# Kernel tuning notes

Hardware: AMD Instinct MI355X
Metric: run time of the kernel (lower is better)

Reference implementation:

```python
import jax, jax.numpy as jnp
import numpy as np

N, E = 50000, 1600000
IN_DIM, HID, L, H = 300, 256, 3, 4
HD = HID // H  # 64
EPS = 1e-5


def setup_inputs() -> dict:
    key = jax.random.key(0)
    ks = jax.random.split(key, 24)
    s = 0.02
    inp = {
        'node_feats': jax.random.normal(ks[0], (N, IN_DIM), jnp.float32),
        'role': jax.random.randint(ks[1], (N,), 0, 3),
        'edge_src': jax.random.randint(ks[2], (E,), 0, N),
        'edge_dst': jax.random.randint(ks[3], (E,), 0, N),
        'edge_weights': jax.random.uniform(ks[4], (E,), jnp.float32),
        # input role transforms (question / entity / context)
        'Wq': jax.random.normal(ks[5], (IN_DIM, HID), jnp.float32) * s,
        'bq': jnp.zeros((HID,), jnp.float32),
        'We': jax.random.normal(ks[6], (IN_DIM, HID), jnp.float32) * s,
        'be': jnp.zeros((HID,), jnp.float32),
        'Wc': jax.random.normal(ks[7], (IN_DIM, HID), jnp.float32) * s,
        'bc': jnp.zeros((HID,), jnp.float32),
        # per-head value projections [H, HID, HD] (q/k projections omitted:
        # softmax over a scalar == 1.0, so they never affect output or grads)
        'Wv': jax.random.normal(ks[8], (H, HID, HD), jnp.float32) * s,
        'bv': jnp.zeros((H, HD), jnp.float32),
        # shared 'default' edge-type transform (the torch code always falls
        # through to 'default' because edata['rel'] entries are tensors)
        'Wd': jax.random.normal(ks[9], (HD, HD), jnp.float32) * s,
        'bd': jnp.zeros((HD,), jnp.float32),
        # attention_output
        'Wo': jax.random.normal(ks[10], (HID, HID), jnp.float32) * s,
        'bo': jnp.zeros((HID,), jnp.float32),
        # GRUCell params (torch layout: [3*HID, in], gate order r,z,n)
        'W_ih': jax.random.normal(ks[11], (3 * HID, HID), jnp.float32) * s,
        'W_hh': jax.random.normal(ks[12], (3 * HID, HID), jnp.float32) * s,
        'b_ih': jnp.zeros((3 * HID,), jnp.float32),
        'b_hh': jnp.zeros((3 * HID,), jnp.float32),
        # per-layer LayerNorm affine params [L, HID]
        'ln_w': jnp.ones((L, HID), jnp.float32),
        'ln_b': jnp.zeros((L, HID), jnp.float32),
    }
    return inp


def _layernorm(x, w, b):
    mu = jnp.mean(x, -1, keepdims=True)
    var = jnp.mean(jnp.square(x - mu), -1, keepdims=True)
    return (x - mu) * jax.lax.rsqrt(var + EPS) * w + b


def _gru_cell(x, hprev, W_ih, W_hh, b_ih, b_hh):
    gi = x @ W_ih.T + b_ih
    gh = hprev @ W_hh.T + b_hh
    i_r, i_z, i_n = jnp.split(gi, 3, axis=-1)
    h_r, h_z, h_n = jnp.split(gh, 3, axis=-1)
    r = jax.nn.sigmoid(i_r + h_r)
    z = jax.nn.sigmoid(i_z + h_z)
    n = jnp.tanh(i_n + r * h_n)
    return (1.0 - z) * n + z * hprev


def reference(node_feats, role, edge_src, edge_dst, edge_weights,
              Wq, bq, We, be, Wc, bc, Wv, bv, Wd, bd, Wo, bo,
              W_ih, W_hh, b_ih, b_hh, ln_w, ln_b):
    n_nodes = node_feats.shape[0]
    # role-dependent input transform: 0=question, 1=evidence/answer, 2=other
    hq = node_feats @ Wq + bq
    he = node_feats @ We + be
    hc = node_feats @ Wc + bc
    r = role[:, None]
    h = jax.nn.relu(jnp.where(r == 0, hq, jnp.where(r == 1, he, hc)))

    path_mem = jax.lax.stop_gradient(h)  # .detach().clone()
    prev_h = h
    num_layers, num_heads = ln_w.shape[0], Wv.shape[0]
    for layer in range(num_layers):
        head_msgs = []
        for hd in range(num_heads):
            # value proj + shared 'default' edge transform (node-level, fused)
            vt = (h @ Wv[hd] + bv[hd]) @ Wd + bd  # [N, HD]
            # scalar softmax == 1.0 -> attn_weight == edge_weight
            msg = vt[edge_src] * edge_weights[:, None]  # [E, HD]
            head_msgs.append(jax.ops.segment_sum(msg, edge_dst,
                                                 num_segments=n_nodes))
        combined = jnp.concatenate(head_msgs, axis=-1)  # [N, HID]
        path_mem = _gru_cell(combined, path_mem, W_ih, W_hh, b_ih, b_hh)
        h = _layernorm(prev_h + combined @ Wo + bo, ln_w[layer], ln_b[layer])
        # dropout: identity in eval mode
        prev_h = h
    return h + path_mem
```

## Files before the change

### kernel.cpp

```cpp
#include <hip/hip_runtime.h>
#include <math.h>

#define NN 50000
#define EE 1600000
#define IND 300
#define KPAD 320
#define NL 3
#define NBLK 785

typedef unsigned short u16;
typedef __attribute__((ext_vector_type(8))) short short8;
typedef __attribute__((ext_vector_type(4))) float floatx4;

__device__ __forceinline__ float b2f(u16 u) {
  union { unsigned i; float f; } v; v.i = ((unsigned)u) << 16; return v.f;
}
__device__ __forceinline__ u16 f2b(float f) {
  union { unsigned i; float f; } v; v.f = f;
  unsigned b = v.i; b += 0x7fffu + ((b >> 16) & 1u);
  return (u16)(b >> 16);
}
__device__ __forceinline__ float sigf(float x) { return 1.0f / (1.0f + __expf(-x)); }

__global__ void count_kernel(const int* __restrict__ dst, int* __restrict__ cnt) {
  int e = blockIdx.x * 256 + threadIdx.x;
  if (e < EE) atomicAdd(&cnt[dst[e]], 1);
}

__global__ void scan_kernel(const int* __restrict__ cnt, int* __restrict__ rs) {
  __shared__ int wsum[16], wpre[16];
  __shared__ int carryS, totS;
  const int t = threadIdx.x;
  const int l = t & 63, wid = t >> 6;
  if (t == 0) carryS = 0;
  __syncthreads();
  for (int base = 0; base < NN; base += 1024) {
    const int carry = carryS;
    const int i = base + t;
    int v = (i < NN) ? cnt[i] : 0;
    int x = v;
    #pragma unroll
    for (int off = 1; off < 64; off <<= 1) {
      int y = __shfl_up(x, off);
      if (l >= off) x += y;
    }
    if (l == 63) wsum[wid] = x;
    __syncthreads();
    if (t < 16) {
      int s = wsum[t];
      int xx = s;
      #pragma unroll
      for (int off = 1; off < 16; off <<= 1) {
        int y = __shfl_up(xx, off);
        if (t >= off) xx += y;
      }
      wpre[t] = xx - s;
      if (t == 15) totS = xx;
    }
    __syncthreads();
    if (i < NN) rs[i] = carry + wpre[wid] + (x - v);
    __syncthreads();
    if (t == 0) carryS = carry + totS;
    __syncthreads();
  }
  if (t == 0) rs[NN] = carryS;
}

__global__ void fill_kernel(const int* __restrict__ dst, const int* __restrict__ rs,
                            int* __restrict__ ncnt, const int* __restrict__ esrc,
                            const float* __restrict__ ew, int2* __restrict__ srcw) {
  int e = blockIdx.x * 256 + threadIdx.x;
  if (e < EE) {
    int d = dst[e];
    int p = atomicAdd(&ncnt[d], 1);
    int2 v;
    v.x = esrc[e];
    v.y = __float_as_int(ew[e]);
    srcw[rs[d] + p] = v;
  }
}

__global__ void role_count(const int* __restrict__ role, int* __restrict__ cnt3) {
  __shared__ int lc[3];
  if (threadIdx.x < 3) lc[threadIdx.x] = 0;
  __syncthreads();
  int i = blockIdx.x * 256 + threadIdx.x;
  if (i < NN) atomicAdd(&lc[role[i]], 1);
  __syncthreads();
  if (threadIdx.x < 3) atomicAdd(&cnt3[threadIdx.x], lc[threadIdx.x]);
}

__global__ void role_plan(const int* __restrict__ cnt3, int* __restrict__ pbase,
                          int* __restrict__ blkrole) {
  __shared__ int pb[4];
  if (threadIdx.x == 0) {
    pb[0] = 0;
    for (int b = 0; b < 3; ++b) pb[b + 1] = pb[b] + (((cnt3[b] + 63) >> 6) << 6);
    for (int b = 0; b < 4; ++b) pbase[b] = pb[b];
  }
  __syncthreads();
  for (int blk = threadIdx.x; blk < NBLK; blk += 256) {
    int m0 = blk * 64;
    int r = -1;
    for (int b = 0; b < 3; ++b)
      if (m0 >= pb[b] && m0 < pb[b + 1]) r = b;
    blkrole[blk] = r;
  }
}

__global__ void role_fill(const int* __restrict__ role, const int* __restrict__ pbase,
                          int* __restrict__ pos3, int* __restrict__ perm) {
  __shared__ int lcnt[3], lbase[3];
  int i = blockIdx.x * 256 + threadIdx.x;
  if (threadIdx.x < 3) lcnt[threadIdx.x] = 0;
  __syncthreads();
  int r = 0, lr = 0;
  bool valid = (i < NN);
  if (valid) {
    r = role[i];
    lr = atomicAdd(&lcnt[r], 1);
  }
  __syncthreads();
  if (threadIdx.x < 3) lbase[threadIdx.x] = atomicAdd(&pos3[threadIdx.x], lcnt[threadIdx.x]);
  __syncthreads();
  if (valid) perm[pbase[r] + lbase[r] + lr] = i;
}

__global__ void xcast_kernel(const float* __restrict__ X, u16* __restrict__ Xb) {
  size_t i = (size_t)blockIdx.x * 256 + threadIdx.x;
  if (i >= (size_t)NN * KPAD) return;
  int r = (int)(i / KPAD), k = (int)(i % KPAD);
  Xb[i] = (k < IND) ? f2b(X[(size_t)r * IND + k]) : (u16)0;
}

__global__ void wt3_kernel(const float* __restrict__ Wq, const float* __restrict__ We,
                           const float* __restrict__ Wc, u16* __restrict__ Wqt,
                           u16* __restrict__ Wet, u16* __restrict__ Wct) {
  int n = blockIdx.x;
  int which = blockIdx.y;
  const float* W = (which == 0) ? Wq : (which == 1) ? We : Wc;
  u16* Wt = (which == 0) ? Wqt : (which == 1) ? Wet : Wct;
  for (int k = threadIdx.x; k < KPAD; k += 256)
    Wt[(size_t)n * KPAD + k] = (k < IND) ? f2b(W[(size_t)k * 256 + n]) : (u16)0;
}

__global__ void wallt_kernel(const float* __restrict__ Wv, const float* __restrict__ Wd,
                             u16* __restrict__ Wallt) {
  int i = blockIdx.x;
  int c = threadIdx.x;
  int hd = c >> 6, j = c & 63;
  const float* wv = &Wv[hd * (256 * 64) + i * 64];
  float s = 0.f;
  #pragma unroll
  for (int m = 0; m < 64; ++m) s = fmaf(wv[m], Wd[m * 64 + j], s);
  Wallt[(size_t)c * 256 + i] = f2b(s);
}

__global__ void ball_kernel(const float* __restrict__ bv, const float* __restrict__ Wd,
                            const float* __restrict__ bd, float* __restrict__ ball) {
  int c = threadIdx.x;
  int hd = c >> 6, j = c & 63;
  float s = bd[j];
  #pragma unroll
  for (int m = 0; m < 64; ++m) s = fmaf(bv[hd * 64 + m], Wd[m * 64 + j], s);
  ball[c] = s;
}

__global__ void wot_kernel(const float* __restrict__ Wo, u16* __restrict__ Wot) {
  int n = blockIdx.x;
  int k = threadIdx.x;
  Wot[(size_t)n * 256 + k] = f2b(Wo[(size_t)k * 256 + n]);
}

__global__ void castbf2_kernel(const float* __restrict__ s0, const float* __restrict__ s1,
                               u16* __restrict__ d0, u16* __restrict__ d1) {
  int i = blockIdx.x * 256 + threadIdx.x;
  const int n = 768 * 256;
  if (i < n) d0[i] = f2b(s0[i]);
  else if (i < 2 * n) d1[i - n] = f2b(s1[i - n]);
}

#define GEMM_PROLOG \
  __shared__ __align__(16) u16 As[64][72]; \
  __shared__ __align__(16) u16 Bs[64][72]; \
  const int t = threadIdx.x; \
  const int lane = t & 63; \
  const int wv_ = t >> 6; \
  const int wr = wv_ >> 1, wc = wv_ & 1; \
  const int l15 = lane & 15, l4 = lane >> 4; \
  const int srow = t >> 2; \
  const int scol = (t & 3) << 4;

#define STAGE_A(AG, ASTRIDE, VALID, ROWIDX, K0) { \
  int4 v0 = {0, 0, 0, 0}, v1 = {0, 0, 0, 0}; \
  if (VALID) { \
    const int4* p_ = (const int4*)&(AG)[(size_t)(ROWIDX) * (ASTRIDE) + (K0) + scol]; \
    v0 = p_[0]; v1 = p_[1]; \
  } \
  *(int4*)&As[srow][scol] = v0; \
  *(int4*)&As[srow][scol + 8] = v1; }

#define STAGE_B(BG, BSTRIDE, ROWIDX, K0) { \
  const int4* p_ = (const int4*)&(BG)[(size_t)(ROWIDX) * (BSTRIDE) + (K0) + scol]; \
  *(int4*)&Bs[srow][scol] = p_[0]; \
  *(int4*)&Bs[srow][scol + 8] = p_[1]; }

#define MFMA_STEP(ACC) { \
  _Pragma("unroll") \
  for (int kc = 0; kc < 2; ++kc) { \
    short8 a0_ = *(const short8*)&As[wr * 32 + 0 + l15][kc * 32 + l4 * 8]; \
    short8 a1_ = *(const short8*)&As[wr * 32 + 16 + l15][kc * 32 + l4 * 8]; \
    short8 b0_ = *(const short8*)&Bs[wc * 32 + 0 + l15][kc * 32 + l4 * 8]; \
    short8 b1_ = *(const short8*)&Bs[wc * 32 + 16 + l15][kc * 32 + l4 * 8]; \
    ACC[0][0] = __builtin_amdgcn_mfma_f32_16x16x32_bf16(a0_, b0_, ACC[0][0], 0, 0, 0); \
    ACC[0][1] = __builtin_amdgcn_mfma_f32_16x16x32_bf16(a0_, b1_, ACC[0][1], 0, 0, 0); \
    ACC[1][0] = __builtin_amdgcn_mfma_f32_16x16x32_bf16(a1_, b0_, ACC[1][0], 0, 0, 0); \
    ACC[1][1] = __builtin_amdgcn_mfma_f32_16x16x32_bf16(a1_, b1_, ACC[1][1], 0, 0, 0); \
  } }

#define GEMM128_PROLOG \
  __shared__ __align__(16) u16 As[128][72]; \
  __shared__ __align__(16) u16 Bs[128][72]; \
  const int t = threadIdx.x; \
  const int lane = t & 63; \
  const int wv_ = t >> 6; \
  const int qr = (wv_ >> 1) * 64, qc = (wv_ & 1) * 64; \
  const int l15 = lane & 15, l4 = lane >> 4; \
  const int srow = t >> 1; \
  const int scol = (t & 1) * 32;

#define STAGE128_A(AG, ASTRIDE, VALID, ROWIDX, K0) { \
  int4 v0 = {0,0,0,0}, v1 = {0,0,0,0}, v2 = {0,0,0,0}, v3 = {0,0,0,0}; \
  if (VALID) { \
    const int4* p_ = (const int4*)&(AG)[(size_t)(ROWIDX) * (ASTRIDE) + (K0) + scol]; \
    v0 = p_[0]; v1 = p_[1]; v2 = p_[2]; v3 = p_[3]; \
  } \
  *(int4*)&As[srow][scol] = v0; *(int4*)&As[srow][scol + 8] = v1; \
  *(int4*)&As[srow][scol + 16] = v2; *(int4*)&As[srow][scol + 24] = v3; }

#define STAGE128_B(BG, BSTRIDE, ROWIDX, K0) { \
  const int4* p_ = (const int4*)&(BG)[(size_t)(ROWIDX) * (BSTRIDE) + (K0) + scol]; \
  *(int4*)&Bs[srow][scol] = p_[0]; *(int4*)&Bs[srow][scol + 8] = p_[1]; \
  *(int4*)&Bs[srow][scol + 16] = p_[2]; *(int4*)&Bs[srow][scol + 24] = p_[3]; }

#define MFMA128_STEP(ACC) { \
  _Pragma("unroll") \
  for (int kc = 0; kc < 2; ++kc) { \
    short8 af_[4], bf_[4]; \
    _Pragma("unroll") \
    for (int m = 0; m < 4; ++m) af_[m] = *(const short8*)&As[qr + m * 16 + l15][kc * 32 + l4 * 8]; \
    _Pragma("unroll") \
    for (int n = 0; n < 4; ++n) bf_[n] = *(const short8*)&Bs[qc + n * 16 + l15][kc * 32 + l4 * 8]; \
    _Pragma("unroll") \
    for (int m = 0; m < 4; ++m) \
      _Pragma("unroll") \
      for (int n = 0; n < 4; ++n) \
        ACC[m][n] = __builtin_amdgcn_mfma_f32_16x16x32_bf16(af_[m], bf_[n], ACC[m][n], 0, 0, 0); \
  } }

__global__ __launch_bounds__(256) void proj_mfma(
    const u16* __restrict__ Xb, const int* __restrict__ perm,
    const int* __restrict__ blkrole,
    const u16* __restrict__ Wqt, const u16* __restrict__ Wet, const u16* __restrict__ Wct,
    const float* __restrict__ bq, const float* __restrict__ be, const float* __restrict__ bc,
    u16* __restrict__ h, u16* __restrict__ pm) {
  const int brole = blkrole[blockIdx.y];
  if (brole < 0) return;
  GEMM_PROLOG
  const int m0 = blockIdx.y * 64;
  const int n0 = blockIdx.x * 64;
  const u16* Bt = (brole == 0) ? Wqt : (brole == 1) ? Wet : Wct;
  const float* bb = (brole == 0) ? bq : (brole == 1) ? be : bc;
  const int prow = perm[m0 + srow];
  floatx4 acc[2][2] = {};
  for (int k0 = 0; k0 < KPAD; k0 += 64) {
    STAGE_A(Xb, KPAD, prow >= 0, prow, k0)
    STAGE_B(Bt, KPAD, n0 + srow, k0)
    __syncthreads();
    MFMA_STEP(acc)
    __syncthreads();
  }
  #pragma unroll
  for (int m = 0; m < 2; ++m)
    #pragma unroll
    for (int reg = 0; reg < 4; ++reg) {
      int gr = m0 + wr * 32 + m * 16 + l4 * 4 + reg;
      int pr = perm[gr];
      if (pr >= 0) {
        #pragma unroll
        for (int n = 0; n < 2; ++n) {
          int c = n0 + wc * 32 + n * 16 + l15;
          float vo = fmaxf(acc[m][n][reg] + bb[c], 0.f);
          u16 ub = f2b(vo);
          h[(size_t)pr * 256 + c] = ub;
          pm[(size_t)pr * 256 + c] = ub;
        }
      }
    }
}

__global__ __launch_bounds__(256) void vgemm_mfma(
    const u16* __restrict__ A, const u16* __restrict__ Bt,
    const float* __restrict__ bias, u16* __restrict__ C) {
  GEMM128_PROLOG
  const int m0 = blockIdx.y * 128;
  const int n0 = blockIdx.x * 128;
  const int ar = m0 + srow;
  floatx4 acc[4][4] = {};
  for (int k0 = 0; k0 < 256; k0 += 64) {
    STAGE128_A(A, 256, ar < NN, ar, k0)
    STAGE128_B(Bt, 256, n0 + srow, k0)
    __syncthreads();
    MFMA128_STEP(acc)
    __syncthreads();
  }
  #pragma unroll
  for (int m = 0; m < 4; ++m)
    #pragma unroll
    for (int reg = 0; reg < 4; ++reg) {
      int gr = m0 + qr + m * 16 + l4 * 4 + reg;
      if (gr < NN) {
        #pragma unroll
        for (int n = 0; n < 4; ++n) {
          int c = n0 + qc + n * 16 + l15;
          C[(size_t)gr * 256 + c] = f2b(acc[m][n][reg] + bias[c]);
        }
      }
    }
}

__global__ __launch_bounds__(256) void agg_kernel(
    const int2* __restrict__ srcw, const int* __restrict__ rs,
    const u16* __restrict__ V, u16* __restrict__ comb) {
  int n = blockIdx.x * 4 + (threadIdx.x >> 6);
  int l = threadIdx.x & 63;
  if (n >= NN) return;
  int s = rs[n], e = rs[n + 1];
  float a0 = 0.f, a1 = 0.f, a2 = 0.f, a3 = 0.f;
  for (int base = s; base < e; base += 64) {
    int2 p = {0, 0};
    if (base + l < e) p = srcw[base + l];
    int cnt = min(64, e - base);
    for (int j = 0; j < cnt; ++j) {
      int src = __shfl(p.x, j);
      float w = __int_as_float(__shfl(p.y, j));
      ushort4 v = *(const ushort4*)&V[(size_t)src * 256 + l * 4];
      a0 = fmaf(w, b2f(v.x), a0);
      a1 = fmaf(w, b2f(v.y), a1);
      a2 = fmaf(w, b2f(v.z), a2);
      a3 = fmaf(w, b2f(v.w), a3);
    }
  }
  ushort4 o;
  o.x = f2b(a0); o.y = f2b(a1); o.z = f2b(a2); o.w = f2b(a3);
  *(ushort4*)&comb[(size_t)n * 256 + l * 4] = o;
}

__global__ __launch_bounds__(256) void grurz_mfma(
    const u16* __restrict__ comb, const u16* __restrict__ pmc,
    const u16* __restrict__ Wiht, const u16* __restrict__ Whht,
    const float* __restrict__ bih, const float* __restrict__ bhh,
    u16* __restrict__ R, u16* __restrict__ Z) {
  GEMM128_PROLOG
  const int m0 = blockIdx.y * 128;
  const int j0 = blockIdx.x * 128;
  const int ar = m0 + srow;
  floatx4 acc[4][4] = {};
  #pragma unroll
  for (int p = 0; p < 2; ++p) {
    const u16* Ag = p ? pmc : comb;
    const u16* Bt = p ? Whht : Wiht;
    for (int k0 = 0; k0 < 256; k0 += 64) {
      STAGE128_A(Ag, 256, ar < NN, ar, k0)
      STAGE128_B(Bt, 256, j0 + srow, k0)
      __syncthreads();
      MFMA128_STEP(acc)
      __syncthreads();
    }
  }
  #pragma unroll
  for (int m = 0; m < 4; ++m)
    #pragma unroll
    for (int reg = 0; reg < 4; ++reg) {
      int gr = m0 + qr + m * 16 + l4 * 4 + reg;
      if (gr < NN) {
        #pragma unroll
        for (int n = 0; n < 4; ++n) {
          int j = j0 + qc + n * 16 + l15;
          float g = sigf(acc[m][n][reg] + bih[j] + bhh[j]);
          if (j < 256) R[(size_t)gr * 256 + j] = f2b(g);
          else         Z[(size_t)gr * 256 + (j - 256)] = f2b(g);
        }
      }
    }
}

__global__ __launch_bounds__(256) void grun_mfma(
    const u16* __restrict__ comb, const u16* __restrict__ pmc,
    const u16* __restrict__ Wiht, const u16* __restrict__ Whht,
    const float* __restrict__ bih, const float* __restrict__ bhh,
    const u16* __restrict__ R, const u16* __restrict__ Z,
    u16* __restrict__ pmn) {
  GEMM128_PROLOG
  const int m0 = blockIdx.y * 128;
  const int n0 = blockIdx.x * 128;
  const int ar = m0 + srow;
  floatx4 ai[4][4] = {};
  floatx4 ah[4][4] = {};
  for (int k0 = 0; k0 < 256; k0 += 64) {
    STAGE128_A(comb, 256, ar < NN, ar, k0)
    STAGE128_B(Wiht, 256, 512 + n0 + srow, k0)
    __syncthreads();
    MFMA128_STEP(ai)
    __syncthreads();
  }
  for (int k0 = 0; k0 < 256; k0 += 64) {
    STAGE128_A(pmc, 256, ar < NN, ar, k0)
    STAGE128_B(Whht, 256, 512 + n0 + srow, k0)
    __syncthreads();
    MFMA128_STEP(ah)
    __syncthreads();
  }
  #pragma unroll
  for (int m = 0; m < 4; ++m)
    #pragma unroll
    for (int reg = 0; reg < 4; ++reg) {
      int gr = m0 + qr + m * 16 + l4 * 4 + reg;
      if (gr < NN) {
        #pragma unroll
        for (int n = 0; n < 4; ++n) {
          int c = n0 + qc + n * 16 + l15;
          float i_n = ai[m][n][reg] + bih[512 + c];
          float h_n = ah[m][n][reg] + bhh[512 + c];
          float rg = b2f(R[(size_t)gr * 256 + c]);
          float z = b2f(Z[(size_t)gr * 256 + c]);
          float po = b2f(pmc[(size_t)gr * 256 + c]);
          float nn2 = tanhf(i_n + rg * h_n);
          pmn[(size_t)gr * 256 + c] = f2b((1.f - z) * nn2 + z * po);
        }
      }
    }
}

__global__ __launch_bounds__(256) void wo_mfma(
    const u16* __restrict__ comb, const u16* __restrict__ Wot,
    const float* __restrict__ bo, const u16* __restrict__ h,
    u16* __restrict__ tmp) {
  GEMM128_PROLOG
  const int m0 = blockIdx.y * 128;
  const int n0 = blockIdx.x * 128;
  const int ar = m0 + srow;
  floatx4 acc[4][4] = {};
  for (int k0 = 0; k0 < 256; k0 += 64) {
    STAGE128_A(comb, 256, ar < NN, ar, k0)
    STAGE128_B(Wot, 256, n0 + srow, k0)
    __syncthreads();
    MFMA128_STEP(acc)
    __syncthreads();
  }
  #pragma unroll
  for (int m = 0; m < 4; ++m)
    #pragma unroll
    for (int reg = 0; reg < 4; ++reg) {
      int gr = m0 + qr + m * 16 + l4 * 4 + reg;
      if (gr < NN) {
        #pragma unroll
        for (int n = 0; n < 4; ++n) {
          int c = n0 + qc + n * 16 + l15;
          float v = acc[m][n][reg] + bo[c] + b2f(h[(size_t)gr * 256 + c]);
          tmp[(size_t)gr * 256 + c] = f2b(v);
        }
      }
    }
}

__global__ __launch_bounds__(256) void ln_kernel(
    const u16* __restrict__ tmp, u16* __restrict__ h,
    const float* __restrict__ lnw, const float* __restrict__ lnb) {
  int n = blockIdx.x * 4 + (threadIdx.x >> 6);
  int l = threadIdx.x & 63;
  if (n >= NN) return;
  ushort4 v = *(const ushort4*)&tmp[(size_t)n * 256 + l * 4];
  float x0 = b2f(v.x), x1 = b2f(v.y), x2 = b2f(v.z), x3 = b2f(v.w);
  float s = x0 + x1 + x2 + x3;
  #pragma unroll
  for (int off = 1; off < 64; off <<= 1) s += __shfl_xor(s, off);
  float mu = s * (1.f / 256.f);
  float d0 = x0 - mu, d1 = x1 - mu, d2 = x2 - mu, d3 = x3 - mu;
  float vs = d0 * d0 + d1 * d1 + d2 * d2 + d3 * d3;
  #pragma unroll
  for (int off = 1; off < 64; off <<= 1) vs += __shfl_xor(vs, off);
  float inv = rsqrtf(vs * (1.f / 256.f) + 1e-5f);
  int c = l * 4;
  ushort4 o;
  o.x = f2b(d0 * inv * lnw[c + 0] + lnb[c + 0]);
  o.y = f2b(d1 * inv * lnw[c + 1] + lnb[c + 1]);
  o.z = f2b(d2 * inv * lnw[c + 2] + lnb[c + 2]);
  o.w = f2b(d3 * inv * lnw[c + 3] + lnb[c + 3]);
  *(ushort4*)&h[(size_t)n * 256 + c] = o;
}

__global__ void add_out(const u16* __restrict__ a, const u16* __restrict__ b,
                        float* __restrict__ o) {
  size_t i = (size_t)blockIdx.x * 256 + threadIdx.x;
  if (i < (size_t)NN * 64) {
    ushort4 x = *(const ushort4*)&a[i * 4];
    ushort4 y = *(const ushort4*)&b[i * 4];
    float4 r;
    r.x = b2f(x.x) + b2f(y.x);
    r.y = b2f(x.y) + b2f(y.y);
    r.z = b2f(x.z) + b2f(y.z);
    r.w = b2f(x.w) + b2f(y.w);
    *(float4*)&o[i * 4] = r;
  }
}

extern "C" void kernel_launch(void* const* d_in, const int* in_sizes, int n_in,
                              void* d_out, int out_size, void* d_ws, size_t ws_size,
                              hipStream_t stream) {
  const float* node_feats = (const float*)d_in[0];
  const int* role = (const int*)d_in[1];
  const int* esrc = (const int*)d_in[2];
  const int* edst = (const int*)d_in[3];
  const float* ew = (const float*)d_in[4];
  const float* Wq = (const float*)d_in[5];
  const float* bq = (const float*)d_in[6];
  const float* We = (const float*)d_in[7];
  const float* be = (const float*)d_in[8];
  const float* Wc = (const float*)d_in[9];
  const float* bc = (const float*)d_in[10];
  const float* Wv = (const float*)d_in[11];
  const float* bv = (const float*)d_in[12];
  const float* Wd = (const float*)d_in[13];
  const float* bd = (const float*)d_in[14];
  const float* Wo = (const float*)d_in[15];
  const float* bo = (const float*)d_in[16];
  const float* Wih = (const float*)d_in[17];
  const float* Whh = (const float*)d_in[18];
  const float* bih = (const float*)d_in[19];
  const float* bhh = (const float*)d_in[20];
  const float* lnw = (const float*)d_in[21];
  const float* lnb = (const float*)d_in[22];
  float* out = (float*)d_out;

  char* ws = (char*)d_ws;
  size_t off = 0;
  auto take = [&](size_t bytes) {
    char* p = ws + off;
    off = (off + bytes + 511) & ~(size_t)511;
    return p;
  };
  const size_t NC2 = (size_t)NN * 256 * 2;
  u16* Xb = (u16*)take((size_t)NN * KPAD * 2);
  u16* h = (u16*)take(NC2);
  u16* pm0 = (u16*)take(NC2);
  u16* pm1 = (u16*)take(NC2);
  u16* V = (u16*)take(NC2);
  u16* comb = (u16*)take(NC2);
  u16* Z = (u16*)take(NC2);
  u16* tmp = (u16*)take(NC2);
  u16* Wqt = (u16*)take((size_t)256 * KPAD * 2);
  u16* Wet = (u16*)take((size_t)256 * KPAD * 2);
  u16* Wct = (u16*)take((size_t)256 * KPAD * 2);
  u16* Wallt = (u16*)take((size_t)256 * 256 * 2);
  u16* Wot = (u16*)take((size_t)256 * 256 * 2);
  u16* Wiht = (u16*)take((size_t)768 * 256 * 2);
  u16* Whht = (u16*)take((size_t)768 * 256 * 2);
  float* ball = (float*)take(256 * 4);
  int* cnt = (int*)take((size_t)NN * 4);
  int* rs = (int*)take((size_t)(NN + 1) * 4);
  int* ncnt = (int*)take((size_t)NN * 4);
  int2* srcw = (int2*)take((size_t)EE * 8);
  int* cnt3 = (int*)take(16);
  int* pos3 = (int*)take(16);
  int* pbase = (int*)take(16);
  int* blkrole = (int*)take((size_t)NBLK * 4);
  int* perm = (int*)take((size_t)NBLK * 64 * 4);
  u16* R = V;

  hipMemsetAsync(cnt, 0, (size_t)NN * 4, stream);
  hipMemsetAsync(ncnt, 0, (size_t)NN * 4, stream);
  hipMemsetAsync(cnt3, 0, 16, stream);
  hipMemsetAsync(pos3, 0, 16, stream);
  hipMemsetAsync(perm, 0xFF, (size_t)NBLK * 64 * 4, stream);

  count_kernel<<<(EE + 255) / 256, 256, 0, stream>>>(edst, cnt);
  scan_kernel<<<1, 1024, 0, stream>>>(cnt, rs);
  fill_kernel<<<(EE + 255) / 256, 256, 0, stream>>>(edst, rs, ncnt, esrc, ew, srcw);

  role_count<<<(NN + 255) / 256, 256, 0, stream>>>(role, cnt3);
  role_plan<<<1, 256, 0, stream>>>(cnt3, pbase, blkrole);
  role_fill<<<(NN + 255) / 256, 256, 0, stream>>>(role, pbase, pos3, perm);

  xcast_kernel<<<(int)(((size_t)NN * KPAD + 255) / 256), 256, 0, stream>>>(node_feats, Xb);
  wt3_kernel<<<dim3(256, 3), 256, 0, stream>>>(Wq, We, Wc, Wqt, Wet, Wct);
  wallt_kernel<<<256, 256, 0, stream>>>(Wv, Wd, Wallt);
  ball_kernel<<<1, 256, 0, stream>>>(bv, Wd, bd, ball);
  wot_kernel<<<256, 256, 0, stream>>>(Wo, Wot);
  castbf2_kernel<<<(2 * 768 * 256 + 255) / 256, 256, 0, stream>>>(Wih, Whh, Wiht, Whht);

  proj_mfma<<<dim3(4, NBLK), 256, 0, stream>>>(Xb, perm, blkrole, Wqt, Wet, Wct,
                                               bq, be, bc, h, pm0);

  u16* pmc = pm0;
  u16* pmn = pm1;
  const int MB128 = (NN + 127) / 128;
  for (int layer = 0; layer < NL; ++layer) {
    vgemm_mfma<<<dim3(2, MB128), 256, 0, stream>>>(h, Wallt, ball, V);
    agg_kernel<<<(NN + 3) / 4, 256, 0, stream>>>(srcw, rs, V, comb);
    grurz_mfma<<<dim3(4, MB128), 256, 0, stream>>>(comb, pmc, Wiht, Whht, bih, bhh, R, Z);
    grun_mfma<<<dim3(2, MB128), 256, 0, stream>>>(comb, pmc, Wiht, Whht, bih, bhh, R, Z, pmn);
    wo_mfma<<<dim3(2, MB128), 256, 0, stream>>>(comb, Wot, bo, h, tmp);
    ln_kernel<<<(NN + 3) / 4, 256, 0, stream>>>(tmp, h, lnw + layer * 256, lnb + layer * 256);
    u16* sw = pmc; pmc = pmn; pmn = sw;
  }

  add_out<<<(int)(((size_t)NN * 64 + 255) / 256), 256, 0, stream>>>(h, pmc, out);
}
```

Before: 1.275 ms.

## Parallelize CSR scan, unroll gather aggregation, fuse final layernorm with output add

Replaces the single-block serial prefix scan with a three-kernel multi-block scan (block-local scan, block-sum scan, add offsets). Unrolls the edge-gather loop in the aggregation kernel by four, using two accumulator sets so more independent loads are in flight. Fuses the last layer's layernorm with the final h + path_mem add, removing one kernel launch and one round trip of h through memory. Adds two kernel launches for the scan and slightly more register pressure in aggregation.

```diff
diff --git a/kernel.cpp b/kernel.cpp
--- a/kernel.cpp
+++ b/kernel.cpp
@@ -27,43 +27,57 @@
   if (e < EE) atomicAdd(&cnt[dst[e]], 1);
 }
 
-__global__ void scan_kernel(const int* __restrict__ cnt, int* __restrict__ rs) {
-  __shared__ int wsum[16], wpre[16];
-  __shared__ int carryS, totS;
-  const int t = threadIdx.x;
-  const int l = t & 63, wid = t >> 6;
-  if (t == 0) carryS = 0;
+__global__ __launch_bounds__(256) void scan1_kernel(const int* __restrict__ cnt,
+                                                    int* __restrict__ rs,
+                                                    int* __restrict__ bsum) {
+  __shared__ int ws[4];
+  const int t = threadIdx.x, l = t & 63, w = t >> 6;
+  const int base = blockIdx.x * 2048 + t * 8;
+  int v[8];
+  int tot = 0;
+  #pragma unroll
+  for (int k = 0; k < 8; ++k) {
+    int i = base + k;
+    v[k] = (i < NN) ? cnt[i] : 0;
+    tot += v[k];
+  }
+  int x = tot;
+  #pragma unroll
+  for (int off = 1; off < 64; off <<= 1) {
+    int y = __shfl_up(x, off);
+    if (l >= off) x += y;
+  }
+  if (l == 63) ws[w] = x;
   __syncthreads();
-  for (int base = 0; base < NN; base += 1024) {
-    const int carry = carryS;
-    const int i = base + t;
-    int v = (i < NN) ? cnt[i] : 0;
-    int x = v;
-    #pragma unroll
-    for (int off = 1; off < 64; off <<= 1) {
-      int y = __shfl_up(x, off);
-      if (l >= off) x += y;
-    }
-    if (l == 63) wsum[wid] = x;
-    __syncthreads();
-    if (t < 16) {
-      int s = wsum[t];
-      int xx = s;
-      #pragma unroll
-      for (int off = 1; off < 16; off <<= 1) {
-        int y = __shfl_up(xx, off);
-        if (t >= off) xx += y;
-      }
-      wpre[t] = xx - s;
-      if (t == 15) totS = xx;
-    }
-    __syncthreads();
-    if (i < NN) rs[i] = carry + wpre[wid] + (x - v);
-    __syncthreads();
-    if (t == 0) carryS = carry + totS;
-    __syncthreads();
-  }
-  if (t == 0) rs[NN] = carryS;
+  int wpre = 0;
+  for (int q = 0; q < w; ++q) wpre += ws[q];
+  int run = wpre + (x - tot);
+  #pragma unroll
+  for (int k = 0; k < 8; ++k) {
+    int i = base + k;
+    if (i < NN) rs[i] = run;
+    run += v[k];
+  }
+  if (t == 255) bsum[blockIdx.x] = wpre + x;
+}
+
+__global__ void scan2_kernel(int* __restrict__ bsum, int nb) {
+  int l = threadIdx.x;
+  int v = (l < nb) ? bsum[l] : 0;
+  int x = v;
+  #pragma unroll
+  for (int off = 1; off < 64; off <<= 1) {
+    int y = __shfl_up(x, off);
+    if (l >= off) x += y;
+  }
+  if (l < nb) bsum[l] = x - v;
+  if (l == 63) bsum[nb] = x;
+}
+
+__global__ void scan3_kernel(const int* __restrict__ bsum, int* __restrict__ rs, int nb) {
+  int i = blockIdx.x * 256 + threadIdx.x;
+  if (i < NN) rs[i] += bsum[i >> 11];
+  if (i == 0) rs[NN] = bsum[nb];
 }
 
 __global__ void fill_kernel(const int* __restrict__ dst, const int* __restrict__ rs,
@@ -337,23 +351,45 @@
   if (n >= NN) return;
   int s = rs[n], e = rs[n + 1];
   float a0 = 0.f, a1 = 0.f, a2 = 0.f, a3 = 0.f;
+  float c0 = 0.f, c1 = 0.f, c2 = 0.f, c3 = 0.f;
+  const size_t loff = (size_t)l * 4;
   for (int base = s; base < e; base += 64) {
     int2 p = {0, 0};
     if (base + l < e) p = srcw[base + l];
     int cnt = min(64, e - base);
-    for (int j = 0; j < cnt; ++j) {
+    int j = 0;
+    for (; j + 4 <= cnt; j += 4) {
+      int s0 = __shfl(p.x, j + 0), s1 = __shfl(p.x, j + 1);
+      int s2 = __shfl(p.x, j + 2), s3 = __shfl(p.x, j + 3);
+      float w0 = __int_as_float(__shfl(p.y, j + 0));
+      float w1 = __int_as_float(__shfl(p.y, j + 1));
+      float w2 = __int_as_float(__shfl(p.y, j + 2));
+      float w3 = __int_as_float(__shfl(p.y, j + 3));
+      ushort4 v0 = *(const ushort4*)&V[(size_t)s0 * 256 + loff];
+      ushort4 v1 = *(const ushort4*)&V[(size_t)s1 * 256 + loff];
+      ushort4 v2 = *(const ushort4*)&V[(size_t)s2 * 256 + loff];
+      ushort4 v3 = *(const ushort4*)&V[(size_t)s3 * 256 + loff];
+      a0 = fmaf(w0, b2f(v0.x), a0); a1 = fmaf(w0, b2f(v0.y), a1);
+      a2 = fmaf(w0, b2f(v0.z), a2); a3 = fmaf(w0, b2f(v0.w), a3);
+      c0 = fmaf(w1, b2f(v1.x), c0); c1 = fmaf(w1, b2f(v1.y), c1);
+      c2 = fmaf(w1, b2f(v1.z), c2); c3 = fmaf(w1, b2f(v1.w), c3);
+      a0 = fmaf(w2, b2f(v2.x), a0); a1 = fmaf(w2, b2f(v2.y), a1);
+      a2 = fmaf(w2, b2f(v2.z), a2); a3 = fmaf(w2, b2f(v2.w), a3);
+      c0 = fmaf(w3, b2f(v3.x), c0); c1 = fmaf(w3, b2f(v3.y), c1);
+      c2 = fmaf(w3, b2f(v3.z), c2); c3 = fmaf(w3, b2f(v3.w), c3);
+    }
+    for (; j < cnt; ++j) {
       int src = __shfl(p.x, j);
       float w = __int_as_float(__shfl(p.y, j));
-      ushort4 v = *(const ushort4*)&V[(size_t)src * 256 + l * 4];
-      a0 = fmaf(w, b2f(v.x), a0);
-      a1 = fmaf(w, b2f(v.y), a1);
-      a2 = fmaf(w, b2f(v.z), a2);
-      a3 = fmaf(w, b2f(v.w), a3);
-    }
-  }
+      ushort4 v = *(const ushort4*)&V[(size_t)src * 256 + loff];
+      a0 = fmaf(w, b2f(v.x), a0); a1 = fmaf(w, b2f(v.y), a1);
+      a2 = fmaf(w, b2f(v.z), a2); a3 = fmaf(w, b2f(v.w), a3);
+    }
+  }
+  a0 += c0; a1 += c1; a2 += c2; a3 += c3;
   ushort4 o;
   o.x = f2b(a0); o.y = f2b(a1); o.z = f2b(a2); o.w = f2b(a3);
-  *(ushort4*)&comb[(size_t)n * 256 + l * 4] = o;
+  *(ushort4*)&comb[(size_t)n * 256 + loff] = o;
 }
 
 __global__ __launch_bounds__(256) void grurz_mfma(
@@ -500,19 +536,32 @@
   *(ushort4*)&h[(size_t)n * 256 + c] = o;
 }
 
-__global__ void add_out(const u16* __restrict__ a, const u16* __restrict__ b,
-                        float* __restrict__ o) {
-  size_t i = (size_t)blockIdx.x * 256 + threadIdx.x;
-  if (i < (size_t)NN * 64) {
-    ushort4 x = *(const ushort4*)&a[i * 4];
-    ushort4 y = *(const ushort4*)&b[i * 4];
-    float4 r;
-    r.x = b2f(x.x) + b2f(y.x);
-    r.y = b2f(x.y) + b2f(y.y);
-    r.z = b2f(x.z) + b2f(y.z);
-    r.w = b2f(x.w) + b2f(y.w);
-    *(float4*)&o[i * 4] = r;
-  }
+__global__ __launch_bounds__(256) void ln_final_kernel(
+    const u16* __restrict__ tmp, const u16* __restrict__ pm,
+    const float* __restrict__ lnw, const float* __restrict__ lnb,
+    float* __restrict__ out) {
+  int n = blockIdx.x * 4 + (threadIdx.x >> 6);
+  int l = threadIdx.x & 63;
+  if (n >= NN) return;
+  ushort4 v = *(const ushort4*)&tmp[(size_t)n * 256 + l * 4];
+  float x0 = b2f(v.x), x1 = b2f(v.y), x2 = b2f(v.z), x3 = b2f(v.w);
+  float s = x0 + x1 + x2 + x3;
+  #pragma unroll
+  for (int off = 1; off < 64; off <<= 1) s += __shfl_xor(s, off);
+  float mu = s * (1.f / 256.f);
+  float d0 = x0 - mu, d1 = x1 - mu, d2 = x2 - mu, d3 = x3 - mu;
+  float vs = d0 * d0 + d1 * d1 + d2 * d2 + d3 * d3;
+  #pragma unroll
+  for (int off = 1; off < 64; off <<= 1) vs += __shfl_xor(vs, off);
+  float inv = rsqrtf(vs * (1.f / 256.f) + 1e-5f);
+  int c = l * 4;
+  ushort4 pv = *(const ushort4*)&pm[(size_t)n * 256 + c];
+  float4 o;
+  o.x = b2f(f2b(d0 * inv * lnw[c + 0] + lnb[c + 0])) + b2f(pv.x);
+  o.y = b2f(f2b(d1 * inv * lnw[c + 1] + lnb[c + 1])) + b2f(pv.y);
+  o.z = b2f(f2b(d2 * inv * lnw[c + 2] + lnb[c + 2])) + b2f(pv.z);
+  o.w = b2f(f2b(d3 * inv * lnw[c + 3] + lnb[c + 3])) + b2f(pv.w);
+  *(float4*)&out[(size_t)n * 256 + c] = o;
 }
 
 extern "C" void kernel_launch(void* const* d_in, const int* in_sizes, int n_in,
@@ -576,7 +625,10 @@
   int* pbase = (int*)take(16);
   int* blkrole = (int*)take((size_t)NBLK * 4);
   int* perm = (int*)take((size_t)NBLK * 64 * 4);
+  int* bsum = (int*)take(64 * 4);
   u16* R = V;
+
+  const int NB_SCAN = (NN + 2047) / 2048;
 
   hipMemsetAsync(cnt, 0, (size_t)NN * 4, stream);
   hipMemsetAsync(ncnt, 0, (size_t)NN * 4, stream);
@@ -585,7 +637,9 @@
   hipMemsetAsync(perm, 0xFF, (size_t)NBLK * 64 * 4, stream);
 
   count_kernel<<<(EE + 255) / 256, 256, 0, stream>>>(edst, cnt);
-  scan_kernel<<<1, 1024, 0, stream>>>(cnt, rs);
+  scan1_kernel<<<NB_SCAN, 256, 0, stream>>>(cnt, rs, bsum);
+  scan2_kernel<<<1, 64, 0, stream>>>(bsum, NB_SCAN);
+  scan3_kernel<<<(NN + 255) / 256, 256, 0, stream>>>(bsum, rs, NB_SCAN);
   fill_kernel<<<(EE + 255) / 256, 256, 0, stream>>>(edst, rs, ncnt, esrc, ew, srcw);
 
   role_count<<<(NN + 255) / 256, 256, 0, stream>>>(role, cnt3);
@@ -611,9 +665,12 @@
     grurz_mfma<<<dim3(4, MB128), 256, 0, stream>>>(comb, pmc, Wiht, Whht, bih, bhh, R, Z);
     grun_mfma<<<dim3(2, MB128), 256, 0, stream>>>(comb, pmc, Wiht, Whht, bih, bhh, R, Z, pmn);
     wo_mfma<<<dim3(2, MB128), 256, 0, stream>>>(comb, Wot, bo, h, tmp);
-    ln_kernel<<<(NN + 3) / 4, 256, 0, stream>>>(tmp, h, lnw + layer * 256, lnb + layer * 256);
+    if (layer < NL - 1) {
+      ln_kernel<<<(NN + 3) / 4, 256, 0, stream>>>(tmp, h, lnw + layer * 256, lnb + layer * 256);
+    } else {
+      ln_final_kernel<<<(NN + 3) / 4, 256, 0, stream>>>(tmp, pmn, lnw + layer * 256,
+                                                        lnb + layer * 256, out);
+    }
     u16* sw = pmc; pmc = pmn; pmn = sw;
   }
-
-  add_out<<<(int)(((size_t)NN * 64 + 255) / 256), 256, 0, stream>>>(h, pmc, out);
-}
+}
```

New measurement: 1.190 ms. -6.6%, faster.
